# Optimization experiments

Hardware: AMD Instinct MI355X
Metric: run time of the kernel (lower is better)

The kernel has to match this reference:

```python
import jax, jax.numpy as jnp
import numpy as np

N = 20000   # nodes per graph
E = 320000  # edges per graph
D_IN, D_H = 128, 304


def _param(key, shape, fan_in):
    return jax.random.normal(key, shape, dtype=jnp.float32) / np.sqrt(fan_in)


def setup_inputs() -> dict:
    key = jax.random.key(0)
    ks = jax.random.split(key, 20)
    inp = {}
    for i, name in enumerate(['x1', 'x2', 'x3']):
        inp[name] = jax.random.normal(ks[i], (N, D_IN), dtype=jnp.float32)
    for i, name in enumerate(['src1', 'dst1', 'src2', 'dst2', 'src3', 'dst3']):
        inp[name] = jax.random.randint(ks[3 + i], (E,), 0, N, dtype=jnp.int32)
    # shared GraphConv weights (DGL GraphConv: h = norm_agg(x) @ W + b)
    inp['W1'] = _param(ks[9], (D_IN, D_H), D_IN)
    inp['b1'] = jnp.zeros((D_H,), jnp.float32)
    inp['W2'] = _param(ks[10], (D_H, D_H), D_H)
    inp['b2'] = jnp.zeros((D_H,), jnp.float32)
    inp['W3'] = _param(ks[11], (D_H, D_H), D_H)
    inp['b3'] = jnp.zeros((D_H,), jnp.float32)
    # MLP head: 304 -> 128 -> 64 -> 1
    inp['fW1'] = _param(ks[12], (D_H, 128), D_H)
    inp['fb1'] = jnp.zeros((128,), jnp.float32)
    inp['fW2'] = _param(ks[13], (128, 64), 128)
    inp['fb2'] = jnp.zeros((64,), jnp.float32)
    inp['fW3'] = _param(ks[14], (64, 1), 64)
    inp['fb3'] = jnp.zeros((1,), jnp.float32)
    return inp


def gcn_conv(x, src, dst, W, b):
    # DGL GraphConv, norm='both': h = D_in^{-1/2} A D_out^{-1/2} x W + b
    ones = jnp.ones((src.shape[0],), x.dtype)
    out_deg = jnp.clip(jax.ops.segment_sum(ones, src, num_segments=N), 1.0)
    in_deg = jnp.clip(jax.ops.segment_sum(ones, dst, num_segments=N), 1.0)
    h = x * jax.lax.rsqrt(out_deg)[:, None]
    agg = jax.ops.segment_sum(h[src], dst, num_segments=N)  # [N, d] SpMM
    agg = agg * jax.lax.rsqrt(in_deg)[:, None]
    return agg @ W + b


def reference(x1, x2, x3, src1, dst1, src2, dst2, src3, dst3,
              W1, b1, W2, b2, W3, b3, fW1, fb1, fW2, fb2, fW3, fb3):
    def branch(x, src, dst):
        x = jax.nn.relu(gcn_conv(x, src, dst, W1, b1))
        x = jax.nn.relu(gcn_conv(x, src, dst, W2, b2))
        x = jax.nn.relu(gcn_conv(x, src, dst, W3, b3))
        return x

    h1 = branch(x1, src1, dst1)
    h2 = branch(x2, src2, dst2)
    h3 = branch(x3, src3, dst3)
    # multi_graph_opt='max': max over all nodes of all three graphs -> [304]
    pooled = jnp.max(jnp.concatenate([h1, h2, h3], axis=0), axis=0)
    # output_opt='fc': MLP head with sigmoid
    z = jax.nn.relu(pooled @ fW1 + fb1)
    z = jax.nn.relu(z @ fW2 + fb2)
    return jax.nn.sigmoid(z @ fW3 + fb3)  # shape [1]
```

## Files before the change

### kernel.cpp

```cpp
#include <hip/hip_runtime.h>
#include <hip/hip_bf16.h>
#include <math.h>

#define NODES 20000
#define EDGES 320000
#define NB 3
#define TOTN (NODES * NB)
#define TOTE (EDGES * NB)
#define D_IN 128
#define D_H 304
#define SCAN_B 59
#define SLICES 40
#define SLICE_E (EDGES / SLICES)
#define ZX TOTN
#define ZQ (TOTN + 192)
#define FILLB 120
#define PACK1B 1875
#define PREPW1B 240

typedef __attribute__((ext_vector_type(4))) float f32x4;
typedef __attribute__((ext_vector_type(2))) float f32x2;

__device__ __forceinline__ void gload16(const void* g, void* l) {
    __builtin_amdgcn_global_load_lds(
        (const __attribute__((address_space(1))) unsigned*)g,
        (__attribute__((address_space(3))) unsigned*)l, 16, 0, 0);
}

__global__ __launch_bounds__(1024, 1) void k_hist(
    const int* __restrict__ s1, const int* __restrict__ d1,
    const int* __restrict__ s2, const int* __restrict__ d2,
    const int* __restrict__ s3, const int* __restrict__ d3,
    unsigned short* __restrict__ partial_in, unsigned short* __restrict__ partial_out,
    int* __restrict__ gctr) {
    __shared__ unsigned hist[NODES / 2];
    if (blockIdx.x == 0 && blockIdx.y == 0 && threadIdx.x == 0) *gctr = 0;
    int g = blockIdx.x / SLICES, s = blockIdx.x % SLICES;
    bool isOut = (blockIdx.y == 1);
    const int* ep;
    if (isOut) ep = (g == 0) ? s1 : ((g == 1) ? s2 : s3);
    else       ep = (g == 0) ? d1 : ((g == 1) ? d2 : d3);
    ep += s * SLICE_E;
    for (int i = threadIdx.x; i < NODES / 2; i += 1024) hist[i] = 0;
    __syncthreads();
    const int4* ep4 = (const int4*)ep;
    for (int i = threadIdx.x; i < SLICE_E / 4; i += 1024) {
        int4 v = ep4[i];
        atomicAdd(&hist[v.x >> 1], 1u << ((v.x & 1) << 4));
        atomicAdd(&hist[v.y >> 1], 1u << ((v.y & 1) << 4));
        atomicAdd(&hist[v.z >> 1], 1u << ((v.z & 1) << 4));
        atomicAdd(&hist[v.w >> 1], 1u << ((v.w & 1) << 4));
    }
    __syncthreads();
    unsigned* po = (unsigned*)((isOut ? partial_out : partial_in) + (size_t)blockIdx.x * NODES);
    for (int i = threadIdx.x; i < NODES / 2; i += 1024) po[i] = hist[i];
}

__global__ void k_degscan(const unsigned short* __restrict__ partial_in,
                          const unsigned short* __restrict__ partial_out,
                          float* __restrict__ inv_in, float* __restrict__ inv_out,
                          int* __restrict__ row_ptr, int* __restrict__ rend,
                          int* __restrict__ O, int* __restrict__ gctr) {
    __shared__ int wsum[16];
    __shared__ int sbase;
    int b = blockIdx.x, t = threadIdx.x;
    int i = b * 1024 + t;
    int lane = t & 63, wid = t >> 6;
    int v = 0;
    int g = 0, ln = 0;
    if (i < TOTN) {
        g = i / NODES; ln = i - g * NODES;
        const unsigned short* pi = partial_in + (size_t)g * SLICES * NODES + ln;
        const unsigned short* po = partial_out + (size_t)g * SLICES * NODES + ln;
        int ci = 0, co = 0;
        #pragma unroll
        for (int s = 0; s < SLICES; s++) { ci += pi[s * NODES]; co += po[s * NODES]; }
        v = ci;
        inv_in[i]  = 1.0f / sqrtf((float)max(ci, 1));
        inv_out[i] = 1.0f / sqrtf((float)max(co, 1));
    }
    int sv = v;
    #pragma unroll
    for (int o = 1; o < 64; o <<= 1) {
        int u = __shfl_up(sv, o, 64);
        if (lane >= o) sv += u;
    }
    if (lane == 63) wsum[wid] = sv;
    __syncthreads();
    if (t < 16) {
        int w = wsum[t];
        #pragma unroll
        for (int o = 1; o < 16; o <<= 1) {
            int u = __shfl_up(w, o, 16);
            if (t >= o) w += u;
        }
        wsum[t] = w;
    }
    __syncthreads();
    if (t == 0) sbase = atomicAdd(gctr, wsum[15]);
    __syncthreads();
    int wbase = (wid > 0) ? wsum[wid - 1] : 0;
    if (i < TOTN) {
        int rp = sbase + wbase + sv - v;
        row_ptr[i] = rp;
        rend[i] = rp + v;
        const unsigned short* pi = partial_in + (size_t)g * SLICES * NODES + ln;
        int* on = O + (size_t)g * SLICES * NODES + ln;
        int run = rp;
        #pragma unroll
        for (int s = 0; s < SLICES; s++) {
            on[s * NODES] = run;
            run += pi[s * NODES];
        }
    }
}

__global__ __launch_bounds__(1024, 1) void k_fillprep(
    const int* __restrict__ s1, const int* __restrict__ d1,
    const int* __restrict__ s2, const int* __restrict__ d2,
    const int* __restrict__ s3, const int* __restrict__ d3,
    const int* __restrict__ O, int* __restrict__ csr,
    const float4* __restrict__ x1, const float4* __restrict__ x2,
    const float4* __restrict__ x3, const float* __restrict__ inv_out,
    unsigned* __restrict__ q,
    const float* __restrict__ W1, const float* __restrict__ W2,
    const float* __restrict__ W3,
    unsigned char* __restrict__ Wt1, unsigned char* __restrict__ Wt2,
    unsigned char* __restrict__ Wt3,
    int* __restrict__ csr_slack, unsigned* __restrict__ x8z,
    unsigned* __restrict__ q8z, int* __restrict__ pooled) {
    __shared__ int cur[NODES];
    int b = blockIdx.x;
    if (b < FILLB) {
        int g = b / SLICES, s = b % SLICES;
        const int* sp = (g == 0) ? s1 : ((g == 1) ? s2 : s3);
        const int* dp = (g == 0) ? d1 : ((g == 1) ? d2 : d3);
        sp += s * SLICE_E; dp += s * SLICE_E;
        const int* on = O + (size_t)b * NODES;
        for (int i = threadIdx.x; i < NODES; i += 1024) cur[i] = on[i];
        __syncthreads();
        int base = g * NODES;
        const int4* sp4 = (const int4*)sp;
        const int4* dp4 = (const int4*)dp;
        for (int i = threadIdx.x; i < SLICE_E / 4; i += 1024) {
            int4 dv = dp4[i];
            int4 sv = sp4[i];
            int p0 = atomicAdd(&cur[dv.x], 1); csr[p0] = sv.x + base;
            int p1 = atomicAdd(&cur[dv.y], 1); csr[p1] = sv.y + base;
            int p2 = atomicAdd(&cur[dv.z], 1); csr[p2] = sv.z + base;
            int p3 = atomicAdd(&cur[dv.w], 1); csr[p3] = sv.w + base;
        }
    } else if (b < FILLB + PACK1B) {
        const int per = NODES * D_IN / 4;
        int i = (b - FILLB) * 1024 + threadIdx.x;
        const float4* s; int j;
        if (i < per)          { s = x1; j = i; }
        else if (i < 2 * per) { s = x2; j = i - per; }
        else                  { s = x3; j = i - 2 * per; }
        float4 v = s[j];
        float sc = inv_out[i >> 5];
        int p = __builtin_amdgcn_cvt_pk_fp8_f32(v.x * sc, v.y * sc, 0, false);
        p = __builtin_amdgcn_cvt_pk_fp8_f32(v.z * sc, v.w * sc, p, true);
        q[i] = (unsigned)p;
    } else if (b < FILLB + PACK1B + PREPW1B) {
        const int N1 = 320 * 128, N2 = 320 * 320;
        int id = (b - FILLB - PACK1B) * 1024 + threadIdx.x;
        const float* W; unsigned char* Wt; int K, Kpad, lid;
        if (id < N1)                { W = W1; Wt = Wt1; K = 128; Kpad = 128; lid = id; }
        else if (id < N1 + N2)      { W = W2; Wt = Wt2; K = 304; Kpad = 320; lid = id - N1; }
        else                        { W = W3; Wt = Wt3; K = 304; Kpad = 320; lid = id - N1 - N2; }
        int n = lid / Kpad, k = lid - n * Kpad;
        unsigned char v = 0;
        if (k < K && n < D_H) {
            float w = W[k * D_H + n];
            v = (unsigned char)(__builtin_amdgcn_cvt_pk_fp8_f32(w, w, 0, false) & 0xff);
        }
        Wt[lid] = v;
    } else {
        int ex = threadIdx.x;
        if (ex < 32) csr_slack[ex] = 0;
        else if (ex < 64) x8z[ex - 32] = 0;
        else if (ex < 144) q8z[ex - 64] = 0;
        else if (ex < 464) pooled[ex - 144] = 0;
    }
}

__global__ void k_spmm_l1(const uint2* __restrict__ h, unsigned char* __restrict__ agg,
                          const int* __restrict__ row_ptr, const int* __restrict__ rend,
                          const int* __restrict__ csr,
                          const float* __restrict__ inv_in) {
    int n = blockIdx.x * 4 + (threadIdx.x >> 6);
    int lane = threadIdx.x & 63;
    int s = lane >> 4;
    int off = lane & 15;
    f32x2 a[4];
    #pragma unroll
    for (int j = 0; j < 4; j++) a[j] = (f32x2){0.f, 0.f};
    int k0 = row_ptr[n], k1 = rend[n];
    int deg = k1 - k0;
    const int* cp = csr + k0 + s;
    int e[8];
    #pragma unroll
    for (int j = 0; j < 8; j++) {
        int ev = cp[4 * j];
        e[j] = (s + 4 * j < deg) ? ev : ZX;
    }
    uint2 u[8];
    #pragma unroll
    for (int j = 0; j < 8; j++)
        if (4 * j < deg) u[j] = h[(size_t)e[j] * 16 + off];
    #pragma unroll
    for (int j = 0; j < 8; j++) {
        if (4 * j < deg) {
            a[0] += __builtin_amdgcn_cvt_pk_f32_fp8(u[j].x, false);
            a[1] += __builtin_amdgcn_cvt_pk_f32_fp8(u[j].x, true);
            a[2] += __builtin_amdgcn_cvt_pk_f32_fp8(u[j].y, false);
            a[3] += __builtin_amdgcn_cvt_pk_f32_fp8(u[j].y, true);
        }
    }
    for (int k = k0 + 32 + s; k < k1; k += 4) {
        int e0 = csr[k];
        uint2 u0 = h[(size_t)e0 * 16 + off];
        a[0] += __builtin_amdgcn_cvt_pk_f32_fp8(u0.x, false);
        a[1] += __builtin_amdgcn_cvt_pk_f32_fp8(u0.x, true);
        a[2] += __builtin_amdgcn_cvt_pk_f32_fp8(u0.y, false);
        a[3] += __builtin_amdgcn_cvt_pk_f32_fp8(u0.y, true);
    }
    float r[8];
    #pragma unroll
    for (int j = 0; j < 4; j++) {
        #pragma unroll
        for (int c = 0; c < 2; c++) {
            float v = a[j][c];
            r[2 * j + c] = v + __shfl(v, lane + 16, 64)
                             + __shfl(v, lane + 32, 64)
                             + __shfl(v, lane + 48, 64);
        }
    }
    if (lane < 16) {
        float wi = inv_in[n];
        int d0 = __builtin_amdgcn_cvt_pk_fp8_f32(r[0] * wi, r[1] * wi, 0, false);
        d0 = __builtin_amdgcn_cvt_pk_fp8_f32(r[2] * wi, r[3] * wi, d0, true);
        int d1 = __builtin_amdgcn_cvt_pk_fp8_f32(r[4] * wi, r[5] * wi, 0, false);
        d1 = __builtin_amdgcn_cvt_pk_fp8_f32(r[6] * wi, r[7] * wi, d1, true);
        uint2 st; st.x = (unsigned)d0; st.y = (unsigned)d1;
        *(uint2*)(agg + (size_t)n * 128 + lane * 8) = st;
    }
}

__global__ void k_spmm_big(const uint4* __restrict__ h, unsigned char* __restrict__ agg,
                           const int* __restrict__ row_ptr, const int* __restrict__ rend,
                           const int* __restrict__ csr,
                           const float* __restrict__ inv_in) {
    int n = blockIdx.x * 4 + (threadIdx.x >> 6);
    int lane = threadIdx.x & 63;
    int s = lane / 20;
    int off = lane % 20;
    f32x2 a[8];
    #pragma unroll
    for (int j = 0; j < 8; j++) a[j] = (f32x2){0.f, 0.f};
    int k0 = row_ptr[n], k1 = rend[n];
    int deg = k1 - k0;
    int degg = (s < 3) ? deg : 0;
    const int* cp = csr + k0 + s;
    int e[8];
    #pragma unroll
    for (int j = 0; j < 8; j++) {
        int ev = cp[3 * j];
        e[j] = (s + 3 * j < degg) ? ev : ZQ;
    }
    uint4 u[8];
    #pragma unroll
    for (int j = 0; j < 8; j++)
        if (3 * j < deg) u[j] = h[(size_t)e[j] * 20 + off];
    #pragma unroll
    for (int j = 0; j < 8; j++) {
        if (3 * j < deg) {
            a[0] += __builtin_amdgcn_cvt_pk_f32_fp8(u[j].x, false);
            a[1] += __builtin_amdgcn_cvt_pk_f32_fp8(u[j].x, true);
            a[2] += __builtin_amdgcn_cvt_pk_f32_fp8(u[j].y, false);
            a[3] += __builtin_amdgcn_cvt_pk_f32_fp8(u[j].y, true);
            a[4] += __builtin_amdgcn_cvt_pk_f32_fp8(u[j].z, false);
            a[5] += __builtin_amdgcn_cvt_pk_f32_fp8(u[j].z, true);
            a[6] += __builtin_amdgcn_cvt_pk_f32_fp8(u[j].w, false);
            a[7] += __builtin_amdgcn_cvt_pk_f32_fp8(u[j].w, true);
        }
    }
    int k1g = k0 + degg;
    for (int k = k0 + 24 + s; k < k1g; k += 3) {
        int e0 = csr[k];
        uint4 u0 = h[(size_t)e0 * 20 + off];
        a[0] += __builtin_amdgcn_cvt_pk_f32_fp8(u0.x, false);
        a[1] += __builtin_amdgcn_cvt_pk_f32_fp8(u0.x, true);
        a[2] += __builtin_amdgcn_cvt_pk_f32_fp8(u0.y, false);
        a[3] += __builtin_amdgcn_cvt_pk_f32_fp8(u0.y, true);
        a[4] += __builtin_amdgcn_cvt_pk_f32_fp8(u0.z, false);
        a[5] += __builtin_amdgcn_cvt_pk_f32_fp8(u0.z, true);
        a[6] += __builtin_amdgcn_cvt_pk_f32_fp8(u0.w, false);
        a[7] += __builtin_amdgcn_cvt_pk_f32_fp8(u0.w, true);
    }
    float r[16];
    #pragma unroll
    for (int j = 0; j < 8; j++) {
        #pragma unroll
        for (int c = 0; c < 2; c++) {
            float v = a[j][c];
            r[2 * j + c] = v + __shfl(v, lane + 20, 64) + __shfl(v, lane + 40, 64);
        }
    }
    if (lane < 20) {
        float wi = inv_in[n];
        int d0 = __builtin_amdgcn_cvt_pk_fp8_f32(r[0] * wi, r[1] * wi, 0, false);
        d0 = __builtin_amdgcn_cvt_pk_fp8_f32(r[2] * wi, r[3] * wi, d0, true);
        int d1 = __builtin_amdgcn_cvt_pk_fp8_f32(r[4] * wi, r[5] * wi, 0, false);
        d1 = __builtin_amdgcn_cvt_pk_fp8_f32(r[6] * wi, r[7] * wi, d1, true);
        int d2 = __builtin_amdgcn_cvt_pk_fp8_f32(r[8] * wi, r[9] * wi, 0, false);
        d2 = __builtin_amdgcn_cvt_pk_fp8_f32(r[10] * wi, r[11] * wi, d2, true);
        int d3 = __builtin_amdgcn_cvt_pk_fp8_f32(r[12] * wi, r[13] * wi, 0, false);
        d3 = __builtin_amdgcn_cvt_pk_fp8_f32(r[14] * wi, r[15] * wi, d3, true);
        uint4 st; st.x = (unsigned)d0; st.y = (unsigned)d1; st.z = (unsigned)d2; st.w = (unsigned)d3;
        *(uint4*)(agg + (size_t)n * 320 + lane * 16) = st;
    }
}

template <int MODE, int K>
__global__ __launch_bounds__(512, 2) void k_gemm_mfma(
    const unsigned char* __restrict__ A,
    const unsigned char* __restrict__ Wt,
    const float* __restrict__ bias,
    const float* __restrict__ inv_out,
    unsigned char* __restrict__ C8, int* __restrict__ gpool, int M) {
    constexpr int BSZ = 320 * K;
    constexpr int SMSZ = (BSZ + 32768 > 81920) ? BSZ + 32768 : 81920;
    __shared__ char SM[SMSZ];
    char* Bs = SM;
    char* As0 = SM + BSZ;
    int tid = threadIdx.x;
    int wv = tid >> 6, lane = tid & 63;
    int quad = lane >> 4, lrow = lane & 15;
    int bm = blockIdx.x * 256;

    f32x4 acc[2][19];
    #pragma unroll
    for (int r = 0; r < 2; r++)
        #pragma unroll
        for (int t = 0; t < 19; t++) acc[r][t] = (f32x4){0.f, 0.f, 0.f, 0.f};

    int swz = (lrow & 3) ^ (lrow >> 2);
    int hb = (quad & 1) * 8;

    constexpr int CPR = K / 16;
    constexpr int NBC = 320 * CPR;
    #pragma unroll
    for (int j = 0; j < (NBC + 511) / 512; j++) {
        int c = j * 512 + tid;
        if (c < NBC) {
            int row = c / CPR, ws = c - row * CPR;
            int seg = ws >> 2, xc = ws & 3;
            int col = xc ^ (row & 3) ^ ((row >> 2) & 3);
            gload16(Wt + (size_t)row * K + seg * 64 + col * 16, Bs + c * 16);
        }
    }
    #pragma unroll
    for (int j = 0; j < 2; j++) {
        int c = j * 512 + tid;
        int row = c >> 2, xc = c & 3;
        int col = xc ^ (row & 3) ^ ((row >> 2) & 3);
        gload16(A + (size_t)(bm + row) * K + col * 16, As0 + c * 16);
    }
    __syncthreads();

    constexpr int NT = K / 64;
    for (int t = 0; t < NT; t++) {
        const char* Asc = As0 + (t & 1) * 16384;
        if (t + 1 < NT) {
            char* Asn = As0 + ((t + 1) & 1) * 16384;
            int ktn = (t + 1) << 6;
            #pragma unroll
            for (int j = 0; j < 2; j++) {
                int c = j * 512 + tid;
                int row = c >> 2, xc = c & 3;
                int col = xc ^ (row & 3) ^ ((row >> 2) & 3);
                gload16(A + (size_t)(bm + row) * K + ktn + col * 16, Asn + c * 16);
            }
        }
        int kt = t << 6;
        #pragma unroll
        for (int sub = 0; sub < 2; sub++) {
            int c0 = sub * 2 + (quad >> 1);
            int cx = (c0 ^ swz) * 16 + hb;
            int ra = wv * 32 + lrow;
            long long a0 = *(const long long*)(Asc + ra * 64 + cx);
            long long a1 = *(const long long*)(Asc + (ra + 16) * 64 + cx);
            #pragma unroll
            for (int u = 0; u < 19; u++) {
                long long b = *(const long long*)(Bs + (size_t)(u * 16 + lrow) * K + kt + cx);
                acc[0][u] = __builtin_amdgcn_mfma_f32_16x16x32_fp8_fp8(a0, b, acc[0][u], 0, 0, 0);
                acc[1][u] = __builtin_amdgcn_mfma_f32_16x16x32_fp8_fp8(a1, b, acc[1][u], 0, 0, 0);
            }
        }
        __syncthreads();
    }
    if (MODE == 0) {
        unsigned char* OUT = (unsigned char*)SM;
        if (tid < 256) *(uint4*)(OUT + tid * 320 + 304) = make_uint4(0u, 0u, 0u, 0u);
        #pragma unroll
        for (int t = 0; t < 19; t++) {
            int col = t * 16 + lrow;
            float bv = bias[col];
            #pragma unroll
            for (int r = 0; r < 2; r++) {
                int rl = wv * 32 + r * 16 + quad * 4;
                #pragma unroll
                for (int g = 0; g < 4; g++) {
                    int row = bm + rl + g;
                    float sc = inv_out[min(row, M - 1)];
                    float v = fmaxf(acc[r][t][g] + bv, 0.f) * sc;
                    int p = __builtin_amdgcn_cvt_pk_fp8_f32(v, v, 0, false);
                    OUT[(rl + g) * 320 + col] = (unsigned char)(p & 0xff);
                }
            }
        }
        __syncthreads();
        #pragma unroll
        for (int j = 0; j < 10; j++) {
            int c = j * 512 + tid;
            *(uint4*)(C8 + (size_t)bm * 320 + (size_t)c * 16) = *(const uint4*)(OUT + c * 16);
        }
    } else {
        int* pmax = (int*)SM;
        for (int i = tid; i < D_H; i += 512) pmax[i] = 0;
        __syncthreads();
        #pragma unroll
        for (int t = 0; t < 19; t++) {
            int col = t * 16 + lrow;
            float bv = bias[col];
            float m = 0.f;
            #pragma unroll
            for (int r = 0; r < 2; r++) {
                int rbase = bm + wv * 32 + r * 16 + quad * 4;
                #pragma unroll
                for (int g = 0; g < 4; g++) {
                    int row = rbase + g;
                    if (row < M) m = fmaxf(m, fmaxf(acc[r][t][g] + bv, 0.f));
                }
            }
            atomicMax(&pmax[col], __float_as_int(m));
        }
        __syncthreads();
        for (int i = tid; i < D_H; i += 512)
            atomicMax(&gpool[i], pmax[i]);
    }
}

__global__ void k_mlp(const int* __restrict__ pooled_i,
                      const float* __restrict__ fW1, const float* __restrict__ fb1,
                      const float* __restrict__ fW2, const float* __restrict__ fb2,
                      const float* __restrict__ fW3, const float* __restrict__ fb3,
                      float* __restrict__ out) {
    __shared__ float p[D_H];
    __shared__ float z1[128];
    __shared__ float z2[64];
    int t = threadIdx.x;
    if (t < D_H) p[t] = __int_as_float(pooled_i[t]);
    __syncthreads();
    if (t < 128) {
        float acc = fb1[t];
        for (int k = 0; k < D_H; k++) acc += p[k] * fW1[k * 128 + t];
        z1[t] = fmaxf(acc, 0.f);
    }
    __syncthreads();
    if (t < 64) {
        float acc = fb2[t];
        for (int k = 0; k < 128; k++) acc += z1[k] * fW2[k * 64 + t];
        z2[t] = fmaxf(acc, 0.f);
    }
    __syncthreads();
    if (t == 0) {
        float acc = fb3[0];
        for (int k = 0; k < 64; k++) acc += z2[k] * fW3[k];
        out[0] = 1.f / (1.f + expf(-acc));
    }
}

extern "C" void kernel_launch(void* const* d_in, const int* in_sizes, int n_in,
                              void* d_out, int out_size, void* d_ws, size_t ws_size,
                              hipStream_t stream) {
    const float* x1 = (const float*)d_in[0];
    const float* x2 = (const float*)d_in[1];
    const float* x3 = (const float*)d_in[2];
    const int* src1 = (const int*)d_in[3];
    const int* dst1 = (const int*)d_in[4];
    const int* src2 = (const int*)d_in[5];
    const int* dst2 = (const int*)d_in[6];
    const int* src3 = (const int*)d_in[7];
    const int* dst3 = (const int*)d_in[8];
    const float* W1 = (const float*)d_in[9];
    const float* b1 = (const float*)d_in[10];
    const float* W2 = (const float*)d_in[11];
    const float* b2 = (const float*)d_in[12];
    const float* W3 = (const float*)d_in[13];
    const float* b3 = (const float*)d_in[14];
    const float* fW1 = (const float*)d_in[15];
    const float* fb1 = (const float*)d_in[16];
    const float* fW2 = (const float*)d_in[17];
    const float* fb2 = (const float*)d_in[18];
    const float* fW3 = (const float*)d_in[19];
    const float* fb3 = (const float*)d_in[20];
    float* out = (float*)d_out;

    char* w = (char*)d_ws;
    unsigned* X8       = (unsigned*)w;      w += (size_t)(TOTN + 1) * 32 * 4;
    unsigned char* Q8  = (unsigned char*)w; w += (size_t)(TOTN + 320) * 320;
    unsigned char* P8  = (unsigned char*)w; w += (size_t)(TOTN + 320) * 320;
    unsigned char* Wt1 = (unsigned char*)w; w += (size_t)320 * 128;
    unsigned char* Wt2 = (unsigned char*)w; w += (size_t)320 * 320;
    unsigned char* Wt3 = (unsigned char*)w; w += (size_t)320 * 320;
    w = (char*)(((size_t)w + 255) & ~(size_t)255);
    unsigned short* partial_in  = (unsigned short*)w; w += (size_t)NB * SLICES * NODES * 2;
    unsigned short* partial_out = (unsigned short*)w; w += (size_t)NB * SLICES * NODES * 2;
    int* O         = (int*)w;    w += (size_t)NB * SLICES * NODES * 4;
    float* inv_out = (float*)w;  w += (size_t)TOTN * 4;
    float* inv_in  = (float*)w;  w += (size_t)TOTN * 4;
    int* row_ptr   = (int*)w;    w += (size_t)TOTN * 4;
    int* rend      = (int*)w;    w += (size_t)TOTN * 4;
    int* csr       = (int*)w;    w += (size_t)(TOTE + 32) * 4;
    int* pooled    = (int*)w;    w += 320 * 4;
    int* gctr      = (int*)w;    w += 64;

    k_hist<<<dim3(NB * SLICES, 2), 1024, 0, stream>>>(src1, dst1, src2, dst2, src3, dst3,
                                                      partial_in, partial_out, gctr);
    k_degscan<<<SCAN_B, 1024, 0, stream>>>(partial_in, partial_out,
                                           inv_in, inv_out, row_ptr, rend, O, gctr);
    k_fillprep<<<FILLB + PACK1B + PREPW1B + 1, 1024, 0, stream>>>(
        src1, dst1, src2, dst2, src3, dst3, O, csr,
        (const float4*)x1, (const float4*)x2, (const float4*)x3, inv_out, X8,
        W1, W2, W3, Wt1, Wt2, Wt3,
        csr + TOTE, X8 + (size_t)ZX * 32, (unsigned*)(Q8 + (size_t)ZQ * 320), pooled);

    int ggrid = (TOTN + 255) / 256;

    k_spmm_l1<<<TOTN / 4, 256, 0, stream>>>((const uint2*)X8, P8, row_ptr, rend, csr, inv_in);
    k_gemm_mfma<0, 128><<<ggrid, 512, 0, stream>>>(P8, Wt1, b1, inv_out,
                                                   Q8, nullptr, TOTN);
    k_spmm_big<<<TOTN / 4, 256, 0, stream>>>((const uint4*)Q8, P8, row_ptr, rend, csr, inv_in);
    k_gemm_mfma<0, 320><<<ggrid, 512, 0, stream>>>(P8, Wt2, b2, inv_out,
                                                   Q8, nullptr, TOTN);
    k_spmm_big<<<TOTN / 4, 256, 0, stream>>>((const uint4*)Q8, P8, row_ptr, rend, csr, inv_in);
    k_gemm_mfma<1, 320><<<ggrid, 512, 0, stream>>>(P8, Wt3, b3, nullptr,
                                                   nullptr, pooled, TOTN);

    k_mlp<<<1, 320, 0, stream>>>(pooled, fW1, fb1, fW2, fb2, fW3, fb3, out);
}
```

Before: 316.3 us.

## Fuse SpMM aggregation into per-layer GEMM kernels via LDS-resident A tiles

Each GCN layer's sparse aggregation and its dense fp8 MFMA GEMM now run in a single kernel. Each block gathers 128 rows into swizzled LDS and multiplies them there, so the aggregated intermediate is never written to and read back from global memory, and three launches are removed. Layers 2 and 3 double-buffer weight K-slices through LDS. The GEMM M tile drops from 256 to 128, which means more weight reloads per row. Ping-pong output buffers (Q8/R8) and zero padding for row_ptr/rend are added so out-of-range tail rows are handled safely.

```diff
diff --git a/kernel.cpp b/kernel.cpp
--- a/kernel.cpp
+++ b/kernel.cpp
@@ -17,6 +17,7 @@
 #define FILLB 120
 #define PACK1B 1875
 #define PREPW1B 240
+#define GGRID 469
 
 typedef __attribute__((ext_vector_type(4))) float f32x4;
 typedef __attribute__((ext_vector_type(2))) float f32x2;
@@ -128,7 +129,8 @@
     unsigned char* __restrict__ Wt1, unsigned char* __restrict__ Wt2,
     unsigned char* __restrict__ Wt3,
     int* __restrict__ csr_slack, unsigned* __restrict__ x8z,
-    unsigned* __restrict__ q8z, int* __restrict__ pooled) {
+    unsigned* __restrict__ q8z, unsigned* __restrict__ r8z,
+    int* __restrict__ pooled, int* __restrict__ row_ptr, int* __restrict__ rend) {
     __shared__ int cur[NODES];
     int b = blockIdx.x;
     if (b < FILLB) {
@@ -181,249 +183,296 @@
         if (ex < 32) csr_slack[ex] = 0;
         else if (ex < 64) x8z[ex - 32] = 0;
         else if (ex < 144) q8z[ex - 64] = 0;
-        else if (ex < 464) pooled[ex - 144] = 0;
-    }
-}
-
-__global__ void k_spmm_l1(const uint2* __restrict__ h, unsigned char* __restrict__ agg,
-                          const int* __restrict__ row_ptr, const int* __restrict__ rend,
-                          const int* __restrict__ csr,
-                          const float* __restrict__ inv_in) {
-    int n = blockIdx.x * 4 + (threadIdx.x >> 6);
-    int lane = threadIdx.x & 63;
-    int s = lane >> 4;
-    int off = lane & 15;
-    f32x2 a[4];
-    #pragma unroll
-    for (int j = 0; j < 4; j++) a[j] = (f32x2){0.f, 0.f};
-    int k0 = row_ptr[n], k1 = rend[n];
-    int deg = k1 - k0;
-    const int* cp = csr + k0 + s;
-    int e[8];
-    #pragma unroll
-    for (int j = 0; j < 8; j++) {
-        int ev = cp[4 * j];
-        e[j] = (s + 4 * j < deg) ? ev : ZX;
-    }
-    uint2 u[8];
-    #pragma unroll
-    for (int j = 0; j < 8; j++)
-        if (4 * j < deg) u[j] = h[(size_t)e[j] * 16 + off];
-    #pragma unroll
-    for (int j = 0; j < 8; j++) {
-        if (4 * j < deg) {
-            a[0] += __builtin_amdgcn_cvt_pk_f32_fp8(u[j].x, false);
-            a[1] += __builtin_amdgcn_cvt_pk_f32_fp8(u[j].x, true);
-            a[2] += __builtin_amdgcn_cvt_pk_f32_fp8(u[j].y, false);
-            a[3] += __builtin_amdgcn_cvt_pk_f32_fp8(u[j].y, true);
-        }
-    }
-    for (int k = k0 + 32 + s; k < k1; k += 4) {
-        int e0 = csr[k];
-        uint2 u0 = h[(size_t)e0 * 16 + off];
-        a[0] += __builtin_amdgcn_cvt_pk_f32_fp8(u0.x, false);
-        a[1] += __builtin_amdgcn_cvt_pk_f32_fp8(u0.x, true);
-        a[2] += __builtin_amdgcn_cvt_pk_f32_fp8(u0.y, false);
-        a[3] += __builtin_amdgcn_cvt_pk_f32_fp8(u0.y, true);
-    }
-    float r[8];
-    #pragma unroll
-    for (int j = 0; j < 4; j++) {
-        #pragma unroll
-        for (int c = 0; c < 2; c++) {
-            float v = a[j][c];
-            r[2 * j + c] = v + __shfl(v, lane + 16, 64)
-                             + __shfl(v, lane + 32, 64)
-                             + __shfl(v, lane + 48, 64);
-        }
-    }
-    if (lane < 16) {
-        float wi = inv_in[n];
-        int d0 = __builtin_amdgcn_cvt_pk_fp8_f32(r[0] * wi, r[1] * wi, 0, false);
-        d0 = __builtin_amdgcn_cvt_pk_fp8_f32(r[2] * wi, r[3] * wi, d0, true);
-        int d1 = __builtin_amdgcn_cvt_pk_fp8_f32(r[4] * wi, r[5] * wi, 0, false);
-        d1 = __builtin_amdgcn_cvt_pk_fp8_f32(r[6] * wi, r[7] * wi, d1, true);
-        uint2 st; st.x = (unsigned)d0; st.y = (unsigned)d1;
-        *(uint2*)(agg + (size_t)n * 128 + lane * 8) = st;
-    }
-}
-
-__global__ void k_spmm_big(const uint4* __restrict__ h, unsigned char* __restrict__ agg,
-                           const int* __restrict__ row_ptr, const int* __restrict__ rend,
-                           const int* __restrict__ csr,
-                           const float* __restrict__ inv_in) {
-    int n = blockIdx.x * 4 + (threadIdx.x >> 6);
-    int lane = threadIdx.x & 63;
-    int s = lane / 20;
-    int off = lane % 20;
-    f32x2 a[8];
-    #pragma unroll
-    for (int j = 0; j < 8; j++) a[j] = (f32x2){0.f, 0.f};
-    int k0 = row_ptr[n], k1 = rend[n];
-    int deg = k1 - k0;
-    int degg = (s < 3) ? deg : 0;
-    const int* cp = csr + k0 + s;
-    int e[8];
-    #pragma unroll
-    for (int j = 0; j < 8; j++) {
-        int ev = cp[3 * j];
-        e[j] = (s + 3 * j < degg) ? ev : ZQ;
-    }
-    uint4 u[8];
-    #pragma unroll
-    for (int j = 0; j < 8; j++)
-        if (3 * j < deg) u[j] = h[(size_t)e[j] * 20 + off];
-    #pragma unroll
-    for (int j = 0; j < 8; j++) {
-        if (3 * j < deg) {
-            a[0] += __builtin_amdgcn_cvt_pk_f32_fp8(u[j].x, false);
-            a[1] += __builtin_amdgcn_cvt_pk_f32_fp8(u[j].x, true);
-            a[2] += __builtin_amdgcn_cvt_pk_f32_fp8(u[j].y, false);
-            a[3] += __builtin_amdgcn_cvt_pk_f32_fp8(u[j].y, true);
-            a[4] += __builtin_amdgcn_cvt_pk_f32_fp8(u[j].z, false);
-            a[5] += __builtin_amdgcn_cvt_pk_f32_fp8(u[j].z, true);
-            a[6] += __builtin_amdgcn_cvt_pk_f32_fp8(u[j].w, false);
-            a[7] += __builtin_amdgcn_cvt_pk_f32_fp8(u[j].w, true);
-        }
-    }
-    int k1g = k0 + degg;
-    for (int k = k0 + 24 + s; k < k1g; k += 3) {
-        int e0 = csr[k];
-        uint4 u0 = h[(size_t)e0 * 20 + off];
-        a[0] += __builtin_amdgcn_cvt_pk_f32_fp8(u0.x, false);
-        a[1] += __builtin_amdgcn_cvt_pk_f32_fp8(u0.x, true);
-        a[2] += __builtin_amdgcn_cvt_pk_f32_fp8(u0.y, false);
-        a[3] += __builtin_amdgcn_cvt_pk_f32_fp8(u0.y, true);
-        a[4] += __builtin_amdgcn_cvt_pk_f32_fp8(u0.z, false);
-        a[5] += __builtin_amdgcn_cvt_pk_f32_fp8(u0.z, true);
-        a[6] += __builtin_amdgcn_cvt_pk_f32_fp8(u0.w, false);
-        a[7] += __builtin_amdgcn_cvt_pk_f32_fp8(u0.w, true);
-    }
-    float r[16];
-    #pragma unroll
-    for (int j = 0; j < 8; j++) {
-        #pragma unroll
-        for (int c = 0; c < 2; c++) {
-            float v = a[j][c];
-            r[2 * j + c] = v + __shfl(v, lane + 20, 64) + __shfl(v, lane + 40, 64);
-        }
-    }
-    if (lane < 20) {
-        float wi = inv_in[n];
-        int d0 = __builtin_amdgcn_cvt_pk_fp8_f32(r[0] * wi, r[1] * wi, 0, false);
-        d0 = __builtin_amdgcn_cvt_pk_fp8_f32(r[2] * wi, r[3] * wi, d0, true);
-        int d1 = __builtin_amdgcn_cvt_pk_fp8_f32(r[4] * wi, r[5] * wi, 0, false);
-        d1 = __builtin_amdgcn_cvt_pk_fp8_f32(r[6] * wi, r[7] * wi, d1, true);
-        int d2 = __builtin_amdgcn_cvt_pk_fp8_f32(r[8] * wi, r[9] * wi, 0, false);
-        d2 = __builtin_amdgcn_cvt_pk_fp8_f32(r[10] * wi, r[11] * wi, d2, true);
-        int d3 = __builtin_amdgcn_cvt_pk_fp8_f32(r[12] * wi, r[13] * wi, 0, false);
-        d3 = __builtin_amdgcn_cvt_pk_fp8_f32(r[14] * wi, r[15] * wi, d3, true);
-        uint4 st; st.x = (unsigned)d0; st.y = (unsigned)d1; st.z = (unsigned)d2; st.w = (unsigned)d3;
-        *(uint4*)(agg + (size_t)n * 320 + lane * 16) = st;
-    }
-}
-
-template <int MODE, int K>
-__global__ __launch_bounds__(512, 2) void k_gemm_mfma(
-    const unsigned char* __restrict__ A,
-    const unsigned char* __restrict__ Wt,
-    const float* __restrict__ bias,
-    const float* __restrict__ inv_out,
-    unsigned char* __restrict__ C8, int* __restrict__ gpool, int M) {
-    constexpr int BSZ = 320 * K;
-    constexpr int SMSZ = (BSZ + 32768 > 81920) ? BSZ + 32768 : 81920;
-    __shared__ char SM[SMSZ];
+        else if (ex < 224) r8z[ex - 144] = 0;
+        else if (ex < 544) pooled[ex - 224] = 0;
+        else if (ex < 608) row_ptr[TOTN + ex - 544] = 0;
+        else if (ex < 672) rend[TOTN + ex - 608] = 0;
+    }
+}
+
+__global__ __launch_bounds__(512, 2) void k_layer1(
+    const uint2* __restrict__ h, const int* __restrict__ row_ptr,
+    const int* __restrict__ rend, const int* __restrict__ csr,
+    const float* __restrict__ inv_in,
+    const unsigned char* __restrict__ Wt, const float* __restrict__ bias,
+    const float* __restrict__ inv_out, unsigned char* __restrict__ C8, int M) {
+    __shared__ char SM[57344];
     char* Bs = SM;
-    char* As0 = SM + BSZ;
+    char* As = SM + 40960;
     int tid = threadIdx.x;
     int wv = tid >> 6, lane = tid & 63;
     int quad = lane >> 4, lrow = lane & 15;
-    int bm = blockIdx.x * 256;
-
-    f32x4 acc[2][19];
-    #pragma unroll
-    for (int r = 0; r < 2; r++)
-        #pragma unroll
-        for (int t = 0; t < 19; t++) acc[r][t] = (f32x4){0.f, 0.f, 0.f, 0.f};
-
+    int bm = blockIdx.x * 128;
+
+    #pragma unroll
+    for (int j = 0; j < 5; j++) {
+        int c = j * 512 + tid;
+        int row = c >> 3, ws = c & 7;
+        int seg = ws >> 2, xc = ws & 3;
+        int col = xc ^ (row & 3) ^ ((row >> 2) & 3);
+        gload16(Wt + (size_t)row * 128 + seg * 64 + col * 16, Bs + c * 16);
+    }
+
+    int s = lane >> 4;
+    int off = lane & 15;
+    for (int p = 0; p < 16; p++) {
+        int r = wv * 16 + p;
+        int n = bm + r;
+        f32x2 a[4];
+        #pragma unroll
+        for (int j = 0; j < 4; j++) a[j] = (f32x2){0.f, 0.f};
+        int k0 = row_ptr[n], k1 = rend[n];
+        int deg = k1 - k0;
+        const int* cp = csr + k0 + s;
+        int e[8];
+        #pragma unroll
+        for (int j = 0; j < 8; j++) {
+            int ev = cp[4 * j];
+            e[j] = (s + 4 * j < deg) ? ev : ZX;
+        }
+        uint2 u[8];
+        #pragma unroll
+        for (int j = 0; j < 8; j++)
+            if (4 * j < deg) u[j] = h[(size_t)e[j] * 16 + off];
+        #pragma unroll
+        for (int j = 0; j < 8; j++) {
+            if (4 * j < deg) {
+                a[0] += __builtin_amdgcn_cvt_pk_f32_fp8(u[j].x, false);
+                a[1] += __builtin_amdgcn_cvt_pk_f32_fp8(u[j].x, true);
+                a[2] += __builtin_amdgcn_cvt_pk_f32_fp8(u[j].y, false);
+                a[3] += __builtin_amdgcn_cvt_pk_f32_fp8(u[j].y, true);
+            }
+        }
+        for (int k = k0 + 32 + s; k < k1; k += 4) {
+            int e0 = csr[k];
+            uint2 u0 = h[(size_t)e0 * 16 + off];
+            a[0] += __builtin_amdgcn_cvt_pk_f32_fp8(u0.x, false);
+            a[1] += __builtin_amdgcn_cvt_pk_f32_fp8(u0.x, true);
+            a[2] += __builtin_amdgcn_cvt_pk_f32_fp8(u0.y, false);
+            a[3] += __builtin_amdgcn_cvt_pk_f32_fp8(u0.y, true);
+        }
+        float rr[8];
+        #pragma unroll
+        for (int j = 0; j < 4; j++) {
+            #pragma unroll
+            for (int c = 0; c < 2; c++) {
+                float v = a[j][c];
+                rr[2 * j + c] = v + __shfl(v, lane + 16, 64)
+                                  + __shfl(v, lane + 32, 64)
+                                  + __shfl(v, lane + 48, 64);
+            }
+        }
+        if (lane < 16) {
+            float wi = inv_in[min(n, TOTN - 1)];
+            int d0 = __builtin_amdgcn_cvt_pk_fp8_f32(rr[0] * wi, rr[1] * wi, 0, false);
+            d0 = __builtin_amdgcn_cvt_pk_fp8_f32(rr[2] * wi, rr[3] * wi, d0, true);
+            int d1 = __builtin_amdgcn_cvt_pk_fp8_f32(rr[4] * wi, rr[5] * wi, 0, false);
+            d1 = __builtin_amdgcn_cvt_pk_fp8_f32(rr[6] * wi, rr[7] * wi, d1, true);
+            uint2 st; st.x = (unsigned)d0; st.y = (unsigned)d1;
+            int rsw = (r & 3) ^ ((r >> 2) & 3);
+            int byte = r * 128 + ((off >> 3) << 6) + ((((off >> 1) & 3) ^ rsw) << 4)
+                     + ((off & 1) << 3);
+            *(uint2*)(As + byte) = st;
+        }
+    }
+    __syncthreads();
+
+    f32x4 acc[19];
+    #pragma unroll
+    for (int t = 0; t < 19; t++) acc[t] = (f32x4){0.f, 0.f, 0.f, 0.f};
     int swz = (lrow & 3) ^ (lrow >> 2);
     int hb = (quad & 1) * 8;
-
-    constexpr int CPR = K / 16;
-    constexpr int NBC = 320 * CPR;
-    #pragma unroll
-    for (int j = 0; j < (NBC + 511) / 512; j++) {
-        int c = j * 512 + tid;
-        if (c < NBC) {
-            int row = c / CPR, ws = c - row * CPR;
-            int seg = ws >> 2, xc = ws & 3;
-            int col = xc ^ (row & 3) ^ ((row >> 2) & 3);
-            gload16(Wt + (size_t)row * K + seg * 64 + col * 16, Bs + c * 16);
-        }
-    }
-    #pragma unroll
-    for (int j = 0; j < 2; j++) {
-        int c = j * 512 + tid;
-        int row = c >> 2, xc = c & 3;
-        int col = xc ^ (row & 3) ^ ((row >> 2) & 3);
-        gload16(A + (size_t)(bm + row) * K + col * 16, As0 + c * 16);
-    }
-    __syncthreads();
-
-    constexpr int NT = K / 64;
-    for (int t = 0; t < NT; t++) {
-        const char* Asc = As0 + (t & 1) * 16384;
-        if (t + 1 < NT) {
-            char* Asn = As0 + ((t + 1) & 1) * 16384;
-            int ktn = (t + 1) << 6;
-            #pragma unroll
-            for (int j = 0; j < 2; j++) {
-                int c = j * 512 + tid;
-                int row = c >> 2, xc = c & 3;
-                int col = xc ^ (row & 3) ^ ((row >> 2) & 3);
-                gload16(A + (size_t)(bm + row) * K + ktn + col * 16, Asn + c * 16);
-            }
-        }
+    #pragma unroll
+    for (int t = 0; t < 2; t++) {
         int kt = t << 6;
         #pragma unroll
         for (int sub = 0; sub < 2; sub++) {
             int c0 = sub * 2 + (quad >> 1);
             int cx = (c0 ^ swz) * 16 + hb;
-            int ra = wv * 32 + lrow;
-            long long a0 = *(const long long*)(Asc + ra * 64 + cx);
-            long long a1 = *(const long long*)(Asc + (ra + 16) * 64 + cx);
+            int ra = wv * 16 + lrow;
+            long long a0 = *(const long long*)(As + ra * 128 + kt + cx);
             #pragma unroll
             for (int u = 0; u < 19; u++) {
-                long long b = *(const long long*)(Bs + (size_t)(u * 16 + lrow) * K + kt + cx);
-                acc[0][u] = __builtin_amdgcn_mfma_f32_16x16x32_fp8_fp8(a0, b, acc[0][u], 0, 0, 0);
-                acc[1][u] = __builtin_amdgcn_mfma_f32_16x16x32_fp8_fp8(a1, b, acc[1][u], 0, 0, 0);
+                long long bb = *(const long long*)(Bs + (u * 16 + lrow) * 128 + kt + cx);
+                acc[u] = __builtin_amdgcn_mfma_f32_16x16x32_fp8_fp8(a0, bb, acc[u], 0, 0, 0);
+            }
+        }
+    }
+    __syncthreads();
+    unsigned char* OUT = (unsigned char*)SM;
+    if (tid < 128) *(uint4*)(OUT + tid * 320 + 304) = make_uint4(0u, 0u, 0u, 0u);
+    #pragma unroll
+    for (int t = 0; t < 19; t++) {
+        int col = t * 16 + lrow;
+        float bv = bias[col];
+        int rl = wv * 16 + quad * 4;
+        #pragma unroll
+        for (int g = 0; g < 4; g++) {
+            int row = bm + rl + g;
+            float sc = inv_out[min(row, M - 1)];
+            float v = fmaxf(acc[t][g] + bv, 0.f) * sc;
+            int p = __builtin_amdgcn_cvt_pk_fp8_f32(v, v, 0, false);
+            OUT[(rl + g) * 320 + col] = (unsigned char)(p & 0xff);
+        }
+    }
+    __syncthreads();
+    #pragma unroll
+    for (int j = 0; j < 5; j++) {
+        int c = j * 512 + tid;
+        *(uint4*)(C8 + (size_t)bm * 320 + (size_t)c * 16) = *(const uint4*)(OUT + c * 16);
+    }
+}
+
+template <int MODE>
+__global__ __launch_bounds__(512, 2) void k_layer23(
+    const uint4* __restrict__ h, const int* __restrict__ row_ptr,
+    const int* __restrict__ rend, const int* __restrict__ csr,
+    const float* __restrict__ inv_in,
+    const unsigned char* __restrict__ Wt, const float* __restrict__ bias,
+    const float* __restrict__ inv_out, unsigned char* __restrict__ C8,
+    int* __restrict__ gpool, int M) {
+    __shared__ char SM[81920];
+    char* As = SM;
+    char* Bd = SM + 40960;
+    int tid = threadIdx.x;
+    int wv = tid >> 6, lane = tid & 63;
+    int quad = lane >> 4, lrow = lane & 15;
+    int bm = blockIdx.x * 128;
+
+    auto stageB = [&](int buf, int kt) {
+        char* Bb = Bd + buf * 20480;
+        #pragma unroll
+        for (int j = 0; j < 3; j++) {
+            int c = j * 512 + tid;
+            if (c < 1280) {
+                int row = c >> 2, xc = c & 3;
+                int col = xc ^ (row & 3) ^ ((row >> 2) & 3);
+                gload16(Wt + (size_t)row * 320 + kt + col * 16, Bb + c * 16);
+            }
+        }
+    };
+    stageB(0, 0);
+
+    int s = lane / 20;
+    int off = lane % 20;
+    for (int p = 0; p < 16; p++) {
+        int r = wv * 16 + p;
+        int n = bm + r;
+        f32x2 a[8];
+        #pragma unroll
+        for (int j = 0; j < 8; j++) a[j] = (f32x2){0.f, 0.f};
+        int k0 = row_ptr[n], k1 = rend[n];
+        int deg = k1 - k0;
+        int degg = (s < 3) ? deg : 0;
+        const int* cp = csr + k0 + s;
+        int e[8];
+        #pragma unroll
+        for (int j = 0; j < 8; j++) {
+            int ev = cp[3 * j];
+            e[j] = (s + 3 * j < degg) ? ev : ZQ;
+        }
+        uint4 u[8];
+        #pragma unroll
+        for (int j = 0; j < 8; j++)
+            if (3 * j < deg) u[j] = h[(size_t)e[j] * 20 + off];
+        #pragma unroll
+        for (int j = 0; j < 8; j++) {
+            if (3 * j < deg) {
+                a[0] += __builtin_amdgcn_cvt_pk_f32_fp8(u[j].x, false);
+                a[1] += __builtin_amdgcn_cvt_pk_f32_fp8(u[j].x, true);
+                a[2] += __builtin_amdgcn_cvt_pk_f32_fp8(u[j].y, false);
+                a[3] += __builtin_amdgcn_cvt_pk_f32_fp8(u[j].y, true);
+                a[4] += __builtin_amdgcn_cvt_pk_f32_fp8(u[j].z, false);
+                a[5] += __builtin_amdgcn_cvt_pk_f32_fp8(u[j].z, true);
+                a[6] += __builtin_amdgcn_cvt_pk_f32_fp8(u[j].w, false);
+                a[7] += __builtin_amdgcn_cvt_pk_f32_fp8(u[j].w, true);
+            }
+        }
+        int k1g = k0 + degg;
+        for (int k = k0 + 24 + s; k < k1g; k += 3) {
+            int e0 = csr[k];
+            uint4 u0 = h[(size_t)e0 * 20 + off];
+            a[0] += __builtin_amdgcn_cvt_pk_f32_fp8(u0.x, false);
+            a[1] += __builtin_amdgcn_cvt_pk_f32_fp8(u0.x, true);
+            a[2] += __builtin_amdgcn_cvt_pk_f32_fp8(u0.y, false);
+            a[3] += __builtin_amdgcn_cvt_pk_f32_fp8(u0.y, true);
+            a[4] += __builtin_amdgcn_cvt_pk_f32_fp8(u0.z, false);
+            a[5] += __builtin_amdgcn_cvt_pk_f32_fp8(u0.z, true);
+            a[6] += __builtin_amdgcn_cvt_pk_f32_fp8(u0.w, false);
+            a[7] += __builtin_amdgcn_cvt_pk_f32_fp8(u0.w, true);
+        }
+        float rr[16];
+        #pragma unroll
+        for (int j = 0; j < 8; j++) {
+            #pragma unroll
+            for (int c = 0; c < 2; c++) {
+                float v = a[j][c];
+                rr[2 * j + c] = v + __shfl(v, lane + 20, 64) + __shfl(v, lane + 40, 64);
+            }
+        }
+        if (lane < 20) {
+            float wi = inv_in[min(n, TOTN - 1)];
+            int d0 = __builtin_amdgcn_cvt_pk_fp8_f32(rr[0] * wi, rr[1] * wi, 0, false);
+            d0 = __builtin_amdgcn_cvt_pk_fp8_f32(rr[2] * wi, rr[3] * wi, d0, true);
+            int d1 = __builtin_amdgcn_cvt_pk_fp8_f32(rr[4] * wi, rr[5] * wi, 0, false);
+            d1 = __builtin_amdgcn_cvt_pk_fp8_f32(rr[6] * wi, rr[7] * wi, d1, true);
+            int d2 = __builtin_amdgcn_cvt_pk_fp8_f32(rr[8] * wi, rr[9] * wi, 0, false);
+            d2 = __builtin_amdgcn_cvt_pk_fp8_f32(rr[10] * wi, rr[11] * wi, d2, true);
+            int d3 = __builtin_amdgcn_cvt_pk_fp8_f32(rr[12] * wi, rr[13] * wi, 0, false);
+            d3 = __builtin_amdgcn_cvt_pk_fp8_f32(rr[14] * wi, rr[15] * wi, d3, true);
+            uint4 st; st.x = (unsigned)d0; st.y = (unsigned)d1;
+            st.z = (unsigned)d2; st.w = (unsigned)d3;
+            int rsw = (r & 3) ^ ((r >> 2) & 3);
+            int byte = r * 320 + ((off >> 2) << 6) + (((off & 3) ^ rsw) << 4);
+            *(uint4*)(As + byte) = st;
+        }
+    }
+    __syncthreads();
+
+    f32x4 acc[19];
+    #pragma unroll
+    for (int t = 0; t < 19; t++) acc[t] = (f32x4){0.f, 0.f, 0.f, 0.f};
+    int swz = (lrow & 3) ^ (lrow >> 2);
+    int hb = (quad & 1) * 8;
+    #pragma unroll
+    for (int t = 0; t < 5; t++) {
+        if (t < 4) stageB((t + 1) & 1, (t + 1) << 6);
+        const char* Bs = Bd + (t & 1) * 20480;
+        int kt = t << 6;
+        #pragma unroll
+        for (int sub = 0; sub < 2; sub++) {
+            int c0 = sub * 2 + (quad >> 1);
+            int cx = (c0 ^ swz) * 16 + hb;
+            int ra = wv * 16 + lrow;
+            long long a0 = *(const long long*)(As + ra * 320 + kt + cx);
+            #pragma unroll
+            for (int u = 0; u < 19; u++) {
+                long long bb = *(const long long*)(Bs + (u * 16 + lrow) * 64 + cx);
+                acc[u] = __builtin_amdgcn_mfma_f32_16x16x32_fp8_fp8(a0, bb, acc[u], 0, 0, 0);
             }
         }
         __syncthreads();
     }
     if (MODE == 0) {
         unsigned char* OUT = (unsigned char*)SM;
-        if (tid < 256) *(uint4*)(OUT + tid * 320 + 304) = make_uint4(0u, 0u, 0u, 0u);
+        if (tid < 128) *(uint4*)(OUT + tid * 320 + 304) = make_uint4(0u, 0u, 0u, 0u);
         #pragma unroll
         for (int t = 0; t < 19; t++) {
             int col = t * 16 + lrow;
             float bv = bias[col];
+            int rl = wv * 16 + quad * 4;
             #pragma unroll
-            for (int r = 0; r < 2; r++) {
-                int rl = wv * 32 + r * 16 + quad * 4;
-                #pragma unroll
-                for (int g = 0; g < 4; g++) {
-                    int row = bm + rl + g;
-                    float sc = inv_out[min(row, M - 1)];
-                    float v = fmaxf(acc[r][t][g] + bv, 0.f) * sc;
-                    int p = __builtin_amdgcn_cvt_pk_fp8_f32(v, v, 0, false);
-                    OUT[(rl + g) * 320 + col] = (unsigned char)(p & 0xff);
-                }
+            for (int g = 0; g < 4; g++) {
+                int row = bm + rl + g;
+                float sc = inv_out[min(row, M - 1)];
+                float v = fmaxf(acc[t][g] + bv, 0.f) * sc;
+                int p = __builtin_amdgcn_cvt_pk_fp8_f32(v, v, 0, false);
+                OUT[(rl + g) * 320 + col] = (unsigned char)(p & 0xff);
             }
         }
         __syncthreads();
         #pragma unroll
-        for (int j = 0; j < 10; j++) {
+        for (int j = 0; j < 5; j++) {
             int c = j * 512 + tid;
             *(uint4*)(C8 + (size_t)bm * 320 + (size_t)c * 16) = *(const uint4*)(OUT + c * 16);
         }
@@ -436,14 +485,11 @@
             int col = t * 16 + lrow;
             float bv = bias[col];
             float m = 0.f;
+            int rbase = bm + wv * 16 + quad * 4;
             #pragma unroll
-            for (int r = 0; r < 2; r++) {
-                int rbase = bm + wv * 32 + r * 16 + quad * 4;
-                #pragma unroll
-                for (int g = 0; g < 4; g++) {
-                    int row = rbase + g;
-                    if (row < M) m = fmaxf(m, fmaxf(acc[r][t][g] + bv, 0.f));
-                }
+            for (int g = 0; g < 4; g++) {
+                int row = rbase + g;
+                if (row < M) m = fmaxf(m, fmaxf(acc[t][g] + bv, 0.f));
             }
             atomicMax(&pmax[col], __float_as_int(m));
         }
@@ -512,7 +558,7 @@
     char* w = (char*)d_ws;
     unsigned* X8       = (unsigned*)w;      w += (size_t)(TOTN + 1) * 32 * 4;
     unsigned char* Q8  = (unsigned char*)w; w += (size_t)(TOTN + 320) * 320;
-    unsigned char* P8  = (unsigned char*)w; w += (size_t)(TOTN + 320) * 320;
+    unsigned char* R8  = (unsigned char*)w; w += (size_t)(TOTN + 320) * 320;
     unsigned char* Wt1 = (unsigned char*)w; w += (size_t)320 * 128;
     unsigned char* Wt2 = (unsigned char*)w; w += (size_t)320 * 320;
     unsigned char* Wt3 = (unsigned char*)w; w += (size_t)320 * 320;
@@ -522,8 +568,8 @@
     int* O         = (int*)w;    w += (size_t)NB * SLICES * NODES * 4;
     float* inv_out = (float*)w;  w += (size_t)TOTN * 4;
     float* inv_in  = (float*)w;  w += (size_t)TOTN * 4;
-    int* row_ptr   = (int*)w;    w += (size_t)TOTN * 4;
-    int* rend      = (int*)w;    w += (size_t)TOTN * 4;
+    int* row_ptr   = (int*)w;    w += (size_t)(TOTN + 64) * 4;
+    int* rend      = (int*)w;    w += (size_t)(TOTN + 64) * 4;
     int* csr       = (int*)w;    w += (size_t)(TOTE + 32) * 4;
     int* pooled    = (int*)w;    w += 320 * 4;
     int* gctr      = (int*)w;    w += 64;
@@ -536,19 +582,16 @@
         src1, dst1, src2, dst2, src3, dst3, O, csr,
         (const float4*)x1, (const float4*)x2, (const float4*)x3, inv_out, X8,
         W1, W2, W3, Wt1, Wt2, Wt3,
-        csr + TOTE, X8 + (size_t)ZX * 32, (unsigned*)(Q8 + (size_t)ZQ * 320), pooled);
-
-    int ggrid = (TOTN + 255) / 256;
-
-    k_spmm_l1<<<TOTN / 4, 256, 0, stream>>>((const uint2*)X8, P8, row_ptr, rend, csr, inv_in);
-    k_gemm_mfma<0, 128><<<ggrid, 512, 0, stream>>>(P8, Wt1, b1, inv_out,
-                                                   Q8, nullptr, TOTN);
-    k_spmm_big<<<TOTN / 4, 256, 0, stream>>>((const uint4*)Q8, P8, row_ptr, rend, csr, inv_in);
-    k_gemm_mfma<0, 320><<<ggrid, 512, 0, stream>>>(P8, Wt2, b2, inv_out,
-                                                   Q8, nullptr, TOTN);
-    k_spmm_big<<<TOTN / 4, 256, 0, stream>>>((const uint4*)Q8, P8, row_ptr, rend, csr, inv_in);
-    k_gemm_mfma<1, 320><<<ggrid, 512, 0, stream>>>(P8, Wt3, b3, nullptr,
-                                                   nullptr, pooled, TOTN);
+        csr + TOTE, X8 + (size_t)ZX * 32,
+        (unsigned*)(Q8 + (size_t)ZQ * 320), (unsigned*)(R8 + (size_t)ZQ * 320),
+        pooled, row_ptr, rend);
+
+    k_layer1<<<GGRID, 512, 0, stream>>>((const uint2*)X8, row_ptr, rend, csr, inv_in,
+                                        Wt1, b1, inv_out, Q8, TOTN);
+    k_layer23<0><<<GGRID, 512, 0, stream>>>((const uint4*)Q8, row_ptr, rend, csr, inv_in,
+                                            Wt2, b2, inv_out, R8, nullptr, TOTN);
+    k_layer23<1><<<GGRID, 512, 0, stream>>>((const uint4*)R8, row_ptr, rend, csr, inv_in,
+                                            Wt3, b3, nullptr, nullptr, pooled, TOTN);
 
     k_mlp<<<1, 320, 0, stream>>>(pooled, fW1, fb1, fW2, fb2, fW3, fb3, out);
 }
```

New measurement: 421.8 us. 33.4% more time.
